# Optimization experiments

Hardware: AMD Instinct MI355X
Metric: run time of the kernel (lower is better)

## Reference

```python
import jax, jax.numpy as jnp
import numpy as np

OMIC_SIZES = [89, 334, 534, 471, 1510, 482]
N = 8192      # number of WSI patches
DIN = 384     # input patch feature dim
DH = 512      # dim_hidden
H = 256       # SNN hidden dim ('small')
K = 6         # topk


def _leaky(x):
    return jnp.where(x >= 0, x, 0.01 * x)


def _elu(x):
    return jnp.where(x > 0, x, jnp.expm1(x))


def setup_inputs() -> dict:
    key = jax.random.key(0)
    ks = iter(jax.random.split(key, 64))
    d = {}
    for i, s in enumerate(OMIC_SIZES, 1):
        d[f'x_omic{i}'] = jax.random.normal(next(ks), (s,), jnp.float32)
        d[f'sig_w1_{i}'] = jax.random.normal(next(ks), (H, s), jnp.float32) * 0.05
    d['x_path'] = jax.random.normal(next(ks), (N, DIN), jnp.float32)
    d['sig_b1'] = jax.random.normal(next(ks), (6, H), jnp.float32) * 0.05
    d['sig_w2'] = jax.random.normal(next(ks), (6, H, H), jnp.float32) * 0.05
    d['sig_b2'] = jax.random.normal(next(ks), (6, H), jnp.float32) * 0.05
    d['fc1_w'] = jax.random.normal(next(ks), (DH, DIN), jnp.float32) * 0.05
    d['fc1_b'] = jax.random.normal(next(ks), (DH,), jnp.float32) * 0.05
    d['wh_w'] = jax.random.normal(next(ks), (DH, DH), jnp.float32) * 0.05
    d['wh_b'] = jax.random.normal(next(ks), (DH,), jnp.float32) * 0.05
    d['wt_w'] = jax.random.normal(next(ks), (DH, DH), jnp.float32) * 0.05
    d['wt_b'] = jax.random.normal(next(ks), (DH,), jnp.float32) * 0.05
    d['lin1_w'] = jax.random.normal(next(ks), (DH, DH), jnp.float32) * 0.05
    d['lin1_b'] = jax.random.normal(next(ks), (DH,), jnp.float32) * 0.05
    d['lin2_w'] = jax.random.normal(next(ks), (DH, DH), jnp.float32) * 0.05
    d['lin2_b'] = jax.random.normal(next(ks), (DH,), jnp.float32) * 0.05
    d['att_w1'] = jax.random.normal(next(ks), (DH // 2, DH), jnp.float32) * 0.05
    d['att_b1'] = jax.random.normal(next(ks), (DH // 2,), jnp.float32) * 0.05
    d['att_w2'] = jax.random.normal(next(ks), (1, DH // 2), jnp.float32) * 0.05
    d['att_b2'] = jax.random.normal(next(ks), (1,), jnp.float32) * 0.05
    return d


def _forward(x_omic1, x_omic2, x_omic3, x_omic4, x_omic5, x_omic6,
             sig_w1_1, sig_w1_2, sig_w1_3, sig_w1_4, sig_w1_5, sig_w1_6,
             sig_b1, sig_w2, sig_b2, x_path,
             fc1_w, fc1_b, wh_w, wh_b, wt_w, wt_b,
             lin1_w, lin1_b, lin2_w, lin2_b,
             att_w1, att_b1, att_w2, att_b2):
    # --- omic SNN branches (Linear+ELU x2; AlphaDropout is identity at eval) ---
    xo = [x_omic1, x_omic2, x_omic3, x_omic4, x_omic5, x_omic6]
    w1 = [sig_w1_1, sig_w1_2, sig_w1_3, sig_w1_4, sig_w1_5, sig_w1_6]
    eo = []
    for i in range(6):
        h = _elu(xo[i] @ w1[i].T + sig_b1[i])
        h = _elu(h @ sig_w2[i].T + sig_b2[i])
        eo.append(h)
    e_omic = jnp.stack(eo)[:, None, :]            # [6,1,256]

    # --- pathology branch ---
    h = _leaky(x_path @ fc1_w.T + fc1_b)[None]    # [1,N,DH]
    h = (h + h.mean(axis=1, keepdims=True)) * 0.5
    e_h = h @ wh_w.T + wh_b                       # [1,N,DH]
    e_t = h @ wt_w.T + wt_b                       # [1,N,DH]

    logits = (e_h * (DH ** -0.5)) @ jnp.swapaxes(e_t, -2, -1)  # [1,N,N]
    vals, idx = jax.lax.top_k(logits, K)          # [1,N,K]
    p = jax.nn.softmax(vals, axis=2)              # [1,N,K]
    Nb = e_t[0][idx[0]][None]                     # gather neighbors [1,N,K,DH]

    eh_r = p[..., None] * Nb + (1.0 - p)[..., None] * e_h[:, :, None, :]
    gate = jnp.tanh(e_h[:, :, None, :] + eh_r)    # [1,N,K,DH]
    # faithful to einsum('ijkl,ijkm->ijk'): separable sums over l and m
    ka = Nb.sum(-1) * gate.sum(-1)                # [1,N,K]
    kp = jax.nn.softmax(ka, axis=2)
    e_Nh = jnp.einsum('bnk,bnkd->bnd', kp, Nb)    # [1,N,DH]

    s = _leaky((e_h + e_Nh) @ lin1_w.T + lin1_b)
    b = _leaky((e_h * e_Nh) @ lin2_w.T + lin2_b)
    e_h2 = s + b                                  # dropout is identity at eval

    # --- GlobalAttention readout ---
    x = e_h2[0]                                   # [N,DH]
    g = _leaky(x @ att_w1.T + att_b1) @ att_w2.T + att_b2  # [N,1]
    a = jax.nn.softmax(g, axis=0)
    e_g = (a * x).sum(axis=0, keepdims=True)      # [1,DH]
    return e_omic, e_h2, e_g


def reference(x_omic1, x_omic2, x_omic3, x_omic4, x_omic5, x_omic6,
              sig_w1_1, sig_w1_2, sig_w1_3, sig_w1_4, sig_w1_5, sig_w1_6,
              sig_b1, sig_w2, sig_b2, x_path,
              fc1_w, fc1_b, wh_w, wh_b, wt_w, wt_b,
              lin1_w, lin1_b, lin2_w, lin2_b,
              att_w1, att_b1, att_w2, att_b2):
    return _forward(x_omic1, x_omic2, x_omic3, x_omic4, x_omic5, x_omic6,
                    sig_w1_1, sig_w1_2, sig_w1_3, sig_w1_4, sig_w1_5, sig_w1_6,
                    sig_b1, sig_w2, sig_b2, x_path,
                    fc1_w, fc1_b, wh_w, wh_b, wt_w, wt_b,
                    lin1_w, lin1_b, lin2_w, lin2_b,
                    att_w1, att_b1, att_w2, att_b2)
```

## Files before the change

kernel.cpp:

```cpp
#include <hip/hip_runtime.h>
#include <math.h>

typedef unsigned short u16;
typedef unsigned int u32;
typedef __attribute__((ext_vector_type(8))) short s8v;
typedef __attribute__((ext_vector_type(16))) float f16f;

__device__ __forceinline__ float b2f(u16 u){ union{u32 i; float f;} v; v.i=((u32)u)<<16; return v.f; }
__device__ __forceinline__ u16 f2b(float f){ union{float f; u32 i;} v; v.f=f; u32 x=v.i; return (u16)((x + 0x7fffu + ((x>>16)&1u)) >> 16); }
__device__ __forceinline__ float leakyf(float x){ return x>=0.f? x : 0.01f*x; }

#define MFMA32(a,b,c) __builtin_amdgcn_mfma_f32_32x32x16_bf16(a,b,c,0,0,0)

__device__ __forceinline__ void gl_lds16(const void* g, void* l){
    __builtin_amdgcn_global_load_lds(
        (const __attribute__((address_space(1))) u32*)g,
        (__attribute__((address_space(3))) u32*)l, 16, 0, 0);
}

struct OmicArgs {
    const float* x[6];
    const float* w1[6];
    int s[6];
};

__global__ __launch_bounds__(256) void omic_kernel(OmicArgs oa,
        const float* __restrict__ sb1, const float* __restrict__ sw2,
        const float* __restrict__ sb2, float* __restrict__ out)
{
    int br = blockIdx.x;
    int t = threadIdx.x;
    int s = oa.s[br];
    __shared__ float xs[1536];
    __shared__ float h1[256];
    const float* x = oa.x[br];
    for (int i=t;i<s;i+=256) xs[i] = x[i];
    __syncthreads();
    const float* w1r = oa.w1[br] + (size_t)t * s;
    float a = sb1[br*256+t];
    for (int i=0;i<s;++i) a += xs[i]*w1r[i];
    a = a>0.f ? a : expm1f(a);
    h1[t] = a;
    __syncthreads();
    const float* w2r = sw2 + (size_t)br*65536 + (size_t)t*256;
    float a2 = sb2[br*256+t];
    #pragma unroll 4
    for (int i=0;i<256;++i) a2 += h1[i]*w2r[i];
    a2 = a2>0.f ? a2 : expm1f(a2);
    out[br*256+t] = a2;
}

struct WcSeg { const float* s; u16* dh; u16* dl; int n; };
struct WcArgs { WcSeg seg[6]; };

__global__ __launch_bounds__(256) void wconv(WcArgs a)
{
    WcSeg sg = a.seg[blockIdx.y];
    for (int i = blockIdx.x*256 + threadIdx.x; i < sg.n; i += gridDim.x*256){
        float v = sg.s[i];
        u16 hi = f2b(v);
        sg.dh[i] = hi;
        if (sg.dl) sg.dl[i] = f2b(v - b2f(hi));
    }
}

template<int SPLITA, int OUTMODE>
__global__ __launch_bounds__(256,2) void gemm_mfma(
    const float* __restrict__ A, const u16* __restrict__ Wh, const u16* __restrict__ Wl,
    const float* __restrict__ bias,
    float* __restrict__ Cf, u16* __restrict__ Ch, u16* __restrict__ Cl,
    int M, int N, int K)
{
    __shared__ u16 Ash[4096], Asl[4096], Bsh[4096], Bsl[4096];
    int tid = threadIdx.x, w = tid >> 6, lane = tid & 63;
    int l31 = lane & 31, l5 = lane >> 5, lo8 = lane << 3;
    int wr = w >> 1, wc = w & 1;
    int bm = blockIdx.x << 7, bn = blockIdx.y << 7;

    f16f acc[2][2];
    #pragma unroll
    for (int a0=0;a0<2;++a0)
        #pragma unroll
        for (int a1=0;a1<2;++a1)
            #pragma unroll
            for (int e=0;e<16;++e) acc[a0][a1][e] = 0.f;

    for (int k0 = 0; k0 < K; k0 += 32){
        __syncthreads();
        #pragma unroll
        for (int kf = 0; kf < 2; ++kf){
            int kk = k0 + (kf<<4) + (l5<<3);
            const float* ap = A + (size_t)(bm + (w<<5) + l31) * K + kk;
            float4 v0 = *(const float4*)ap;
            float4 v1 = *(const float4*)(ap + 4);
            float vv[8] = {v0.x,v0.y,v0.z,v0.w,v1.x,v1.y,v1.z,v1.w};
            s8v hv, lv;
            #pragma unroll
            for (int j=0;j<8;++j){
                u16 hi = f2b(vv[j]);
                hv[j] = (short)hi;
                if (SPLITA) lv[j] = (short)f2b(vv[j] - b2f(hi));
            }
            int fb = ((w<<1)+kf)<<9;
            *(s8v*)&Ash[fb + lo8] = hv;
            if (SPLITA) *(s8v*)&Asl[fb + lo8] = lv;
            size_t gb = (size_t)(bn + (w<<5) + l31) * K + kk;
            gl_lds16(Wh + gb, &Bsh[fb]);
            if (SPLITA) gl_lds16(Wl + gb, &Bsl[fb]);
        }
        __syncthreads();
        #pragma unroll
        for (int kf = 0; kf < 2; ++kf){
            s8v ah[2], al[2];
            #pragma unroll
            for (int rti=0;rti<2;++rti){
                int fa = (((((wr<<1)+rti)<<1)+kf)<<9) + lo8;
                ah[rti] = *(const s8v*)&Ash[fa];
                if (SPLITA) al[rti] = *(const s8v*)&Asl[fa];
            }
            #pragma unroll
            for (int cti=0;cti<2;++cti){
                int fb = (((((wc<<1)+cti)<<1)+kf)<<9) + lo8;
                s8v bh = *(const s8v*)&Bsh[fb];
                s8v bl;
                if (SPLITA) bl = *(const s8v*)&Bsl[fb];
                #pragma unroll
                for (int rti=0;rti<2;++rti){
                    acc[rti][cti] = MFMA32(ah[rti], bh, acc[rti][cti]);
                    if (SPLITA){
                        acc[rti][cti] = MFMA32(ah[rti], bl, acc[rti][cti]);
                        acc[rti][cti] = MFMA32(al[rti], bh, acc[rti][cti]);
                    }
                }
            }
        }
    }
    #pragma unroll
    for (int cti=0;cti<2;++cti){
        int col = bn + (((wc<<1)+cti)<<5) + l31;
        float bv = bias[col];
        #pragma unroll
        for (int rti=0;rti<2;++rti){
            int rbase = bm + (((wr<<1)+rti)<<5) + (l5<<2);
            #pragma unroll
            for (int g=0;g<4;++g){
                #pragma unroll
                for (int i=0;i<4;++i){
                    int row = rbase + (g<<3) + i;
                    float v = acc[rti][cti][(g<<2)+i] + bv;
                    if (OUTMODE==0){
                        Cf[(size_t)row*N + col] = leakyf(v);
                    } else {
                        u16 hi = f2b(v);
                        Ch[(size_t)row*N + col] = hi;
                        Cl[(size_t)row*N + col] = f2b(v - b2f(hi));
                    }
                }
            }
        }
    }
}

__global__ __launch_bounds__(256,2) void lin12_mfma(
    const u16* __restrict__ EHH, const u16* __restrict__ EHL, const u16* __restrict__ ENH,
    const u16* __restrict__ W1b, const float* __restrict__ B1,
    const u16* __restrict__ W2b, const float* __restrict__ B2,
    float* __restrict__ OUT)
{
    const int K = 512, N = 512;
    __shared__ u16 Ss[4096], Ms[4096], B1s[4096], B2s[4096];
    int tid = threadIdx.x, w = tid >> 6, lane = tid & 63;
    int l31 = lane & 31, l5 = lane >> 5, lo8 = lane << 3;
    int wr = w >> 1, wc = w & 1;
    int bm = blockIdx.x << 7, bn = blockIdx.y << 7;

    f16f acc1[2][2], acc2[2][2];
    #pragma unroll
    for (int a0=0;a0<2;++a0)
        #pragma unroll
        for (int a1=0;a1<2;++a1)
            #pragma unroll
            for (int e=0;e<16;++e){ acc1[a0][a1][e]=0.f; acc2[a0][a1][e]=0.f; }

    for (int k0 = 0; k0 < K; k0 += 32){
        __syncthreads();
        #pragma unroll
        for (int kf = 0; kf < 2; ++kf){
            int kk = k0 + (kf<<4) + (l5<<3);
            size_t go = (size_t)(bm + (w<<5) + l31) * K + kk;
            s8v hv = *(const s8v*)(EHH + go);
            s8v lv = *(const s8v*)(EHL + go);
            s8v nv = *(const s8v*)(ENH + go);
            s8v sv, mv;
            #pragma unroll
            for (int j=0;j<8;++j){
                float e = b2f((u16)hv[j]) + b2f((u16)lv[j]);
                float n = b2f((u16)nv[j]);
                sv[j] = (short)f2b(e + n);
                mv[j] = (short)f2b(e * n);
            }
            int fb = ((w<<1)+kf)<<9;
            *(s8v*)&Ss[fb + lo8] = sv;
            *(s8v*)&Ms[fb + lo8] = mv;
            size_t gb = (size_t)(bn + (w<<5) + l31) * K + kk;
            gl_lds16(W1b + gb, &B1s[fb]);
            gl_lds16(W2b + gb, &B2s[fb]);
        }
        __syncthreads();
        #pragma unroll
        for (int kf = 0; kf < 2; ++kf){
            s8v as[2], am[2];
            #pragma unroll
            for (int rti=0;rti<2;++rti){
                int fa = (((((wr<<1)+rti)<<1)+kf)<<9) + lo8;
                as[rti] = *(const s8v*)&Ss[fa];
                am[rti] = *(const s8v*)&Ms[fa];
            }
            #pragma unroll
            for (int cti=0;cti<2;++cti){
                int fb = (((((wc<<1)+cti)<<1)+kf)<<9) + lo8;
                s8v b1 = *(const s8v*)&B1s[fb];
                s8v b2 = *(const s8v*)&B2s[fb];
                #pragma unroll
                for (int rti=0;rti<2;++rti){
                    acc1[rti][cti] = MFMA32(as[rti], b1, acc1[rti][cti]);
                    acc2[rti][cti] = MFMA32(am[rti], b2, acc2[rti][cti]);
                }
            }
        }
    }
    #pragma unroll
    for (int cti=0;cti<2;++cti){
        int col = bn + (((wc<<1)+cti)<<5) + l31;
        float b1v = B1[col], b2v = B2[col];
        #pragma unroll
        for (int rti=0;rti<2;++rti){
            int rbase = bm + (((wr<<1)+rti)<<5) + (l5<<2);
            #pragma unroll
            for (int g=0;g<4;++g){
                #pragma unroll
                for (int i=0;i<4;++i){
                    int row = rbase + (g<<3) + i;
                    float s1 = leakyf(acc1[rti][cti][(g<<2)+i] + b1v);
                    float s2 = leakyf(acc2[rti][cti][(g<<2)+i] + b2v);
                    OUT[(size_t)row*N + col] = s1 + s2;
                }
            }
        }
    }
}

__global__ __launch_bounds__(256) void colmean(const float* __restrict__ H, float* __restrict__ Mc)
{
    __shared__ float red[256];
    int c=blockIdx.x, t=threadIdx.x;
    float s=0;
    for (int i=t;i<8192;i+=256) s += H[(size_t)i*512 + c];
    red[t]=s; __syncthreads();
    for (int o=128;o>0;o>>=1){ if(t<o) red[t]+=red[t+o]; __syncthreads(); }
    if (t==0) Mc[c] = red[0] * (1.0f/8192.0f);
}

__global__ __launch_bounds__(256) void hupd(float* __restrict__ H, const float* __restrict__ Mc)
{
    int i = blockIdx.x*256 + threadIdx.x;
    H[i] = (H[i] + Mc[i & 511]) * 0.5f;
}

struct TileMem { u16 Ah[8*512]; u16 Al[8*512]; u16 Bh[8*512]; u16 Bl[8*512]; };
struct EpiMem  { float Sc[64*132]; };
union SMemU { TileMem t; EpiMem e; };

__global__ __launch_bounds__(256,3) void logits_topk_mfma(
    const u16* __restrict__ EHH, const u16* __restrict__ EHL,
    const u16* __restrict__ ETH, const u16* __restrict__ ETL,
    float* __restrict__ VALS, int* __restrict__ IDX)
{
    const float scale = 0.04419417382415922f;
    __shared__ SMemU sm;
    int tid = threadIdx.x;
    int bm = blockIdx.x << 7;
    int base = blockIdx.y << 9;
    int w = tid >> 6, lane = tid & 63;
    int l31 = lane & 31, l5 = lane >> 5;
    int wr = w >> 1, wc = w & 1;
    int lo8 = lane << 3;
    int r = tid >> 1, q = tid & 1;

    float tv[6]; int ti[6];
    #pragma unroll
    for (int k=0;k<6;++k){ tv[k]=-INFINITY; ti[k]=0; }

    for (int bnoff = 0; bnoff < 512; bnoff += 128){
        int bn = base + bnoff;
        f16f acc[2][2];
        #pragma unroll
        for (int a0=0;a0<2;++a0)
            #pragma unroll
            for (int a1=0;a1<2;++a1)
                #pragma unroll
                for (int e=0;e<16;++e) acc[a0][a1][e] = 0.f;

        for (int k0 = 0; k0 < 512; k0 += 32){
            __syncthreads();
            #pragma unroll
            for (int kf = 0; kf < 2; ++kf){
                int ksub = k0 + (kf<<4) + (l5<<3);
                size_t ga = (size_t)(bm + (w<<5) + l31) * 512 + ksub;
                gl_lds16(EHH + ga, &sm.t.Ah[((w<<1)+kf)<<9]);
                gl_lds16(EHL + ga, &sm.t.Al[((w<<1)+kf)<<9]);
                size_t gb = (size_t)(bn + (w<<5) + l31) * 512 + ksub;
                gl_lds16(ETH + gb, &sm.t.Bh[((w<<1)+kf)<<9]);
                gl_lds16(ETL + gb, &sm.t.Bl[((w<<1)+kf)<<9]);
            }
            __syncthreads();
            #pragma unroll
            for (int kf = 0; kf < 2; ++kf){
                s8v ah[2], al[2];
                #pragma unroll
                for (int rti=0;rti<2;++rti){
                    int fa = (((((wr<<1)+rti)<<1)+kf)<<9) + lo8;
                    ah[rti] = *(const s8v*)&sm.t.Ah[fa];
                    al[rti] = *(const s8v*)&sm.t.Al[fa];
                }
                #pragma unroll
                for (int cti=0;cti<2;++cti){
                    int fb = (((((wc<<1)+cti)<<1)+kf)<<9) + lo8;
                    s8v bh = *(const s8v*)&sm.t.Bh[fb];
                    s8v bl = *(const s8v*)&sm.t.Bl[fb];
                    #pragma unroll
                    for (int rti=0;rti<2;++rti){
                        acc[rti][cti] = MFMA32(ah[rti], bh, acc[rti][cti]);
                        acc[rti][cti] = MFMA32(ah[rti], bl, acc[rti][cti]);
                        acc[rti][cti] = MFMA32(al[rti], bh, acc[rti][cti]);
                    }
                }
            }
        }
        __syncthreads();
        #pragma unroll
        for (int h = 0; h < 2; ++h){
            if (wc == h){
                #pragma unroll
                for (int cti=0;cti<2;++cti){
                    int colw = ((cti<<5) + l31) * 132 + (wr<<6) + (l5<<2);
                    #pragma unroll
                    for (int rti=0;rti<2;++rti){
                        #pragma unroll
                        for (int g=0;g<4;++g){
                            float4 vv;
                            vv.x = acc[rti][cti][(g<<2)+0]*scale;
                            vv.y = acc[rti][cti][(g<<2)+1]*scale;
                            vv.z = acc[rti][cti][(g<<2)+2]*scale;
                            vv.w = acc[rti][cti][(g<<2)+3]*scale;
                            *(float4*)&sm.e.Sc[colw + (rti<<5) + (g<<3)] = vv;
                        }
                    }
                }
            }
            __syncthreads();
            int cbase = bn + (h<<6) + (q<<5);
            #pragma unroll
            for (int i=0;i<32;++i){
                float v = sm.e.Sc[(((q<<5)+i)*132) + r];
                if (v > tv[5]){
                    tv[5]=v; ti[5]=cbase+i;
                    #pragma unroll
                    for (int u=5;u>0;--u){
                        if (tv[u] > tv[u-1]){
                            float tf=tv[u]; tv[u]=tv[u-1]; tv[u-1]=tf;
                            int tg=ti[u]; ti[u]=ti[u-1]; ti[u-1]=tg;
                        }
                    }
                }
            }
            __syncthreads();
        }
    }
    float* Mv = sm.e.Sc;
    int*   Mi = (int*)sm.e.Sc + 1536;
    #pragma unroll
    for (int k=0;k<6;++k){ Mv[r*12 + q*6 + k] = tv[k]; Mi[r*12 + q*6 + k] = ti[k]; }
    __syncthreads();
    if (tid < 128){
        int row = bm + tid;
        float* mv = &Mv[tid*12];
        int*   mi = &Mi[tid*12];
        unsigned used = 0;
        for (int k=0;k<6;++k){
            float bv=-INFINITY; int bc=0;
            for (int c=0;c<12;++c) if (!((used>>c)&1u) && mv[c] > bv){ bv=mv[c]; bc=c; }
            used |= 1u<<bc;
            VALS[(size_t)row*96 + blockIdx.y*6 + k] = bv;
            IDX [(size_t)row*96 + blockIdx.y*6 + k] = mi[bc];
        }
    }
}

__global__ __launch_bounds__(256) void knn_agg(
    const u16* __restrict__ EHH, const u16* __restrict__ EHL,
    const u16* __restrict__ ETH, const u16* __restrict__ ETL,
    const float* __restrict__ VALS, const int* __restrict__ IDX,
    u16* __restrict__ ENH)
{
    int wave = threadIdx.x >> 6, lane = threadIdx.x & 63;
    int row = (blockIdx.x<<2) + wave;
    size_t vb = (size_t)row*96;
    float v0 = VALS[vb + lane];
    float v1 = (lane < 32) ? VALS[vb + 64 + lane] : -INFINITY;
    int e0 = lane, e1 = 64 + lane;
    float v[6]; int id[6];
    #pragma unroll
    for (int k=0;k<6;++k){
        float cv; int ce;
        if (v0 >= v1){ cv=v0; ce=e0; } else { cv=v1; ce=e1; }
        #pragma unroll
        for (int off=1; off<64; off<<=1){
            float ov = __shfl_xor(cv, off, 64);
            int   oe = __shfl_xor(ce, off, 64);
            if (ov > cv || (ov == cv && oe < ce)){ cv=ov; ce=oe; }
        }
        v[k] = cv;
        id[k] = IDX[vb + ce];
        if (e0 == ce) v0 = -INFINITY;
        if (e1 == ce) v1 = -INFINITY;
    }
    float mx=v[0];
    #pragma unroll
    for (int k=1;k<6;++k) mx=fmaxf(mx,v[k]);
    float p[6], se=0.f;
    #pragma unroll
    for (int k=0;k<6;++k){ p[k]=expf(v[k]-mx); se+=p[k]; }
    float inv=1.f/se;
    #pragma unroll
    for (int k=0;k<6;++k) p[k]*=inv;

    size_t ro = (size_t)row*512;
    float e[8];
    #pragma unroll
    for (int j=0;j<8;++j){ int o = lane + (j<<6); e[j]=b2f(EHH[ro+o])+b2f(EHL[ro+o]); }
    float nb[6][8], sn[6], sg[6];
    #pragma unroll
    for (int k=0;k<6;++k){
        size_t no = (size_t)id[k]*512;
        float s_n=0.f, s_g=0.f;
        #pragma unroll
        for (int j=0;j<8;++j){
            int o = lane + (j<<6);
            float nv = b2f(ETH[no+o])+b2f(ETL[no+o]);
            nb[k][j]=nv;
            s_n += nv;
            float ehr_v = p[k]*nv + (1.f-p[k])*e[j];
            s_g += tanhf(e[j] + ehr_v);
        }
        #pragma unroll
        for (int o=1;o<64;o<<=1){ s_n += __shfl_xor(s_n,o,64); s_g += __shfl_xor(s_g,o,64); }
        sn[k]=s_n; sg[k]=s_g;
    }
    float ka[6];
    #pragma unroll
    for (int k=0;k<6;++k) ka[k]=sn[k]*sg[k];
    float km=ka[0];
    #pragma unroll
    for (int k=1;k<6;++k) km=fmaxf(km,ka[k]);
    float kp[6], ks=0.f;
    #pragma unroll
    for (int k=0;k<6;++k){ kp[k]=expf(ka[k]-km); ks+=kp[k]; }
    float kinv=1.f/ks;
    #pragma unroll
    for (int k=0;k<6;++k) kp[k]*=kinv;
    float o8[8]={0,0,0,0,0,0,0,0};
    #pragma unroll
    for (int k=0;k<6;++k)
        #pragma unroll
        for (int j=0;j<8;++j) o8[j] += kp[k]*nb[k][j];
    #pragma unroll
    for (int j=0;j<8;++j) ENH[ro + lane + (j<<6)] = f2b(o8[j]);
}

__global__ __launch_bounds__(256) void att_g(
    const float* __restrict__ HM, const float* __restrict__ W2,
    const float* __restrict__ B2, float* __restrict__ G)
{
    int wave=threadIdx.x>>6, lane=threadIdx.x&63;
    int row=(blockIdx.x<<2)+wave;
    const float* hr = HM + (size_t)row*256;
    float s=0.f;
    #pragma unroll
    for (int j=0;j<4;++j) s += hr[lane+(j<<6)] * W2[lane+(j<<6)];
    #pragma unroll
    for (int o=1;o<64;o<<=1) s += __shfl_xor(s,o,64);
    if (lane==0) G[row] = s + B2[0];
}

__global__ __launch_bounds__(1024) void softg(float* __restrict__ G)
{
    __shared__ float red[1024];
    __shared__ float MS[2];
    int t=threadIdx.x;
    float m=-INFINITY;
    for (int i=t;i<8192;i+=1024) m=fmaxf(m,G[i]);
    red[t]=m; __syncthreads();
    for (int o=512;o>0;o>>=1){ if(t<o) red[t]=fmaxf(red[t],red[t+o]); __syncthreads(); }
    if (t==0) MS[0]=red[0];
    __syncthreads();
    float M=MS[0], s=0.f;
    for (int i=t;i<8192;i+=1024) s += expf(G[i]-M);
    red[t]=s; __syncthreads();
    for (int o=512;o>0;o>>=1){ if(t<o) red[t]+=red[t+o]; __syncthreads(); }
    if (t==0) MS[1]=red[0];
    __syncthreads();
    float inv=1.f/MS[1];
    for (int i=t;i<8192;i+=1024) G[i] = expf(G[i]-M)*inv;
}

__global__ __launch_bounds__(256) void eg_kernel(
    const float* __restrict__ A, const float* __restrict__ X, float* __restrict__ OUT)
{
    __shared__ float red[256];
    int d = blockIdx.x, t = threadIdx.x;
    float s=0.f;
    for (int i=t;i<8192;i+=256) s += A[i]*X[(size_t)i*512 + d];
    red[t]=s; __syncthreads();
    for (int o=128;o>0;o>>=1){ if(t<o) red[t]+=red[t+o]; __syncthreads(); }
    if (t==0) OUT[d] = red[0];
}

extern "C" void kernel_launch(void* const* d_in, const int* in_sizes, int n_in,
                              void* d_out, int out_size, void* d_ws, size_t ws_size,
                              hipStream_t stream)
{
    (void)n_in; (void)out_size; (void)ws_size;
    static const int ss[6] = {89,334,534,471,1510,482};

    bool sig_order = (in_sizes[12] == 1536);
    OmicArgs oa;
    const float *sb1, *sw2, *sb2, *xpath;
    if (sig_order) {
        for (int i=0;i<6;++i){ oa.x[i]=(const float*)d_in[i]; oa.w1[i]=(const float*)d_in[6+i]; oa.s[i]=ss[i]; }
        sb1   = (const float*)d_in[12];
        sw2   = (const float*)d_in[13];
        sb2   = (const float*)d_in[14];
        xpath = (const float*)d_in[15];
    } else {
        for (int i=0;i<6;++i){ oa.x[i]=(const float*)d_in[2*i]; oa.w1[i]=(const float*)d_in[2*i+1]; oa.s[i]=ss[i]; }
        xpath = (const float*)d_in[12];
        sb1   = (const float*)d_in[13];
        sw2   = (const float*)d_in[14];
        sb2   = (const float*)d_in[15];
    }
    const float* fc1w = (const float*)d_in[16];
    const float* fc1b = (const float*)d_in[17];
    const float* whw  = (const float*)d_in[18];
    const float* whb  = (const float*)d_in[19];
    const float* wtw  = (const float*)d_in[20];
    const float* wtb  = (const float*)d_in[21];
    const float* l1w  = (const float*)d_in[22];
    const float* l1b  = (const float*)d_in[23];
    const float* l2w  = (const float*)d_in[24];
    const float* l2b  = (const float*)d_in[25];
    const float* aw1  = (const float*)d_in[26];
    const float* ab1  = (const float*)d_in[27];
    const float* aw2  = (const float*)d_in[28];
    const float* ab2  = (const float*)d_in[29];

    float* out = (float*)d_out;
    float* eh2 = out + 1536;
    float* egp = out + 1536 + 4194304;

    float* h    = eh2;
    float* vals = eh2;
    int*   idxb = (int*)(eh2 + 786432);

    char* wsb = (char*)d_ws;
    u16* ehh = (u16*)wsb;
    u16* ehl = ehh + 4194304;
    u16* eth = ehl + 4194304;
    u16* etl = eth + 4194304;
    u16* enh = etl + 4194304;
    u16* wreg = enh + 4194304;
    u16* fc1h = wreg,            *fc1l = wreg +  196608;
    u16* whh  = wreg +  393216,  *whl  = wreg +  655360;
    u16* wth  = wreg +  917504,  *wtl  = wreg + 1179648;
    u16* l1bf = wreg + 1441792,  *l2bf = wreg + 1703936;
    u16* awbf = wreg + 1966080;
    float* mcol = (float*)(wsb + 48234496);
    float* gbuf = mcol + 512;
    float* hm   = (float*)eth;

    omic_kernel<<<6,256,0,stream>>>(oa, sb1, sw2, sb2, out);

    WcArgs wa;
    wa.seg[0] = { fc1w, fc1h, fc1l, 196608 };
    wa.seg[1] = { whw,  whh,  whl,  262144 };
    wa.seg[2] = { wtw,  wth,  wtl,  262144 };
    wa.seg[3] = { l1w,  l1bf, nullptr, 262144 };
    wa.seg[4] = { l2w,  l2bf, nullptr, 262144 };
    wa.seg[5] = { aw1,  awbf, nullptr, 131072 };
    wconv<<<dim3(16,6),256,0,stream>>>(wa);

    gemm_mfma<1,0><<<dim3(64,4),256,0,stream>>>(xpath, fc1h, fc1l, fc1b, h, nullptr, nullptr, 8192,512,384);
    colmean<<<512,256,0,stream>>>(h, mcol);
    hupd<<<16384,256,0,stream>>>(h, mcol);
    gemm_mfma<1,1><<<dim3(64,4),256,0,stream>>>(h, whh, whl, whb, nullptr, ehh, ehl, 8192,512,512);
    gemm_mfma<1,1><<<dim3(64,4),256,0,stream>>>(h, wth, wtl, wtb, nullptr, eth, etl, 8192,512,512);
    logits_topk_mfma<<<dim3(64,16),256,0,stream>>>(ehh, ehl, eth, etl, vals, idxb);
    knn_agg<<<2048,256,0,stream>>>(ehh, ehl, eth, etl, vals, idxb, enh);
    lin12_mfma<<<dim3(64,4),256,0,stream>>>(ehh, ehl, enh, l1bf, l1b, l2bf, l2b, eh2);
    gemm_mfma<0,0><<<dim3(64,2),256,0,stream>>>(eh2, awbf, awbf, ab1, hm, nullptr, nullptr, 8192,256,512);
    att_g<<<2048,256,0,stream>>>(hm, aw2, ab2, gbuf);
    softg<<<1,1024,0,stream>>>(gbuf);
    eg_kernel<<<512,256,0,stream>>>(gbuf, eh2, egp);
}
```

Measured before the change: 918.6 us.

## Widen logits tile to 128x256 and halve top-k column splits

The logits+topk kernel now computes 128x256 output tiles (4 column subtiles per wave) and covers 1024 columns per block, so the grid's y dimension drops from 16 to 8. The A fragments are reused across twice as many B columns, which cuts global loads of the row operand. The partial top-k buffer shrinks from 96 to 48 candidates per row, so knn_agg's merge handles a single 48-entry lane set. In exchange, accumulator registers and LDS use roughly double, and occupancy is lowered to 2 blocks per SM.

```diff
diff --git a/kernel.cpp b/kernel.cpp
--- a/kernel.cpp
+++ b/kernel.cpp
@@ -267,11 +267,11 @@
     H[i] = (H[i] + Mc[i & 511]) * 0.5f;
 }
 
-struct TileMem { u16 Ah[8*512]; u16 Al[8*512]; u16 Bh[8*512]; u16 Bl[8*512]; };
+struct TileMem { u16 Ah[4096]; u16 Al[4096]; u16 Bh[8192]; u16 Bl[8192]; };
 struct EpiMem  { float Sc[64*132]; };
 union SMemU { TileMem t; EpiMem e; };
 
-__global__ __launch_bounds__(256,3) void logits_topk_mfma(
+__global__ __launch_bounds__(256,2) void logits_topk_mfma(
     const u16* __restrict__ EHH, const u16* __restrict__ EHL,
     const u16* __restrict__ ETH, const u16* __restrict__ ETL,
     float* __restrict__ VALS, int* __restrict__ IDX)
@@ -280,24 +280,23 @@
     __shared__ SMemU sm;
     int tid = threadIdx.x;
     int bm = blockIdx.x << 7;
-    int base = blockIdx.y << 9;
+    int base = blockIdx.y << 10;
     int w = tid >> 6, lane = tid & 63;
-    int l31 = lane & 31, l5 = lane >> 5;
+    int l31 = lane & 31, l5 = lane >> 5, lo8 = lane << 3;
     int wr = w >> 1, wc = w & 1;
-    int lo8 = lane << 3;
     int r = tid >> 1, q = tid & 1;
 
     float tv[6]; int ti[6];
     #pragma unroll
     for (int k=0;k<6;++k){ tv[k]=-INFINITY; ti[k]=0; }
 
-    for (int bnoff = 0; bnoff < 512; bnoff += 128){
-        int bn = base + bnoff;
-        f16f acc[2][2];
+    for (int bt = 0; bt < 4; ++bt){
+        int bn = base + (bt<<8);
+        f16f acc[2][4];
         #pragma unroll
         for (int a0=0;a0<2;++a0)
             #pragma unroll
-            for (int a1=0;a1<2;++a1)
+            for (int a1=0;a1<4;++a1)
                 #pragma unroll
                 for (int e=0;e<16;++e) acc[a0][a1][e] = 0.f;
 
@@ -305,13 +304,17 @@
             __syncthreads();
             #pragma unroll
             for (int kf = 0; kf < 2; ++kf){
-                int ksub = k0 + (kf<<4) + (l5<<3);
-                size_t ga = (size_t)(bm + (w<<5) + l31) * 512 + ksub;
+                int kk = k0 + (kf<<4) + (l5<<3);
+                size_t ga = (size_t)(bm + (w<<5) + l31) * 512 + kk;
                 gl_lds16(EHH + ga, &sm.t.Ah[((w<<1)+kf)<<9]);
                 gl_lds16(EHL + ga, &sm.t.Al[((w<<1)+kf)<<9]);
-                size_t gb = (size_t)(bn + (w<<5) + l31) * 512 + ksub;
-                gl_lds16(ETH + gb, &sm.t.Bh[((w<<1)+kf)<<9]);
-                gl_lds16(ETL + gb, &sm.t.Bl[((w<<1)+kf)<<9]);
+                #pragma unroll
+                for (int j = 0; j < 2; ++j){
+                    int ct = (w<<1) + j;
+                    size_t gb = (size_t)(bn + (ct<<5) + l31) * 512 + kk;
+                    gl_lds16(ETH + gb, &sm.t.Bh[((ct<<1)+kf)<<9]);
+                    gl_lds16(ETL + gb, &sm.t.Bl[((ct<<1)+kf)<<9]);
+                }
             }
             __syncthreads();
             #pragma unroll
@@ -324,8 +327,8 @@
                     al[rti] = *(const s8v*)&sm.t.Al[fa];
                 }
                 #pragma unroll
-                for (int cti=0;cti<2;++cti){
-                    int fb = (((((wc<<1)+cti)<<1)+kf)<<9) + lo8;
+                for (int cti=0;cti<4;++cti){
+                    int fb = (((((wc<<2)+cti)<<1)+kf)<<9) + lo8;
                     s8v bh = *(const s8v*)&sm.t.Bh[fb];
                     s8v bl = *(const s8v*)&sm.t.Bl[fb];
                     #pragma unroll
@@ -339,11 +342,12 @@
         }
         __syncthreads();
         #pragma unroll
-        for (int h = 0; h < 2; ++h){
-            if (wc == h){
-                #pragma unroll
-                for (int cti=0;cti<2;++cti){
-                    int colw = ((cti<<5) + l31) * 132 + (wr<<6) + (l5<<2);
+        for (int s = 0; s < 4; ++s){
+            if (wc == (s>>1)){
+                #pragma unroll
+                for (int cp=0;cp<2;++cp){
+                    int cti = ((s&1)<<1) + cp;
+                    int colw = ((cp<<5) + l31) * 132 + (wr<<6) + (l5<<2);
                     #pragma unroll
                     for (int rti=0;rti<2;++rti){
                         #pragma unroll
@@ -359,7 +363,7 @@
                 }
             }
             __syncthreads();
-            int cbase = bn + (h<<6) + (q<<5);
+            int cbase = bn + (s<<6) + (q<<5);
             #pragma unroll
             for (int i=0;i<32;++i){
                 float v = sm.e.Sc[(((q<<5)+i)*132) + r];
@@ -391,8 +395,8 @@
             float bv=-INFINITY; int bc=0;
             for (int c=0;c<12;++c) if (!((used>>c)&1u) && mv[c] > bv){ bv=mv[c]; bc=c; }
             used |= 1u<<bc;
-            VALS[(size_t)row*96 + blockIdx.y*6 + k] = bv;
-            IDX [(size_t)row*96 + blockIdx.y*6 + k] = mi[bc];
+            VALS[(size_t)row*48 + blockIdx.y*6 + k] = bv;
+            IDX [(size_t)row*48 + blockIdx.y*6 + k] = mi[bc];
         }
     }
 }
@@ -405,15 +409,13 @@
 {
     int wave = threadIdx.x >> 6, lane = threadIdx.x & 63;
     int row = (blockIdx.x<<2) + wave;
-    size_t vb = (size_t)row*96;
-    float v0 = VALS[vb + lane];
-    float v1 = (lane < 32) ? VALS[vb + 64 + lane] : -INFINITY;
-    int e0 = lane, e1 = 64 + lane;
+    size_t vb = (size_t)row*48;
+    float v0 = (lane < 48) ? VALS[vb + lane] : -INFINITY;
+    int e0 = lane;
     float v[6]; int id[6];
     #pragma unroll
     for (int k=0;k<6;++k){
-        float cv; int ce;
-        if (v0 >= v1){ cv=v0; ce=e0; } else { cv=v1; ce=e1; }
+        float cv = v0; int ce = e0;
         #pragma unroll
         for (int off=1; off<64; off<<=1){
             float ov = __shfl_xor(cv, off, 64);
@@ -423,7 +425,6 @@
         v[k] = cv;
         id[k] = IDX[vb + ce];
         if (e0 == ce) v0 = -INFINITY;
-        if (e1 == ce) v1 = -INFINITY;
     }
     float mx=v[0];
     #pragma unroll
@@ -599,15 +600,19 @@
     wa.seg[5] = { aw1,  awbf, nullptr, 131072 };
     wconv<<<dim3(16,6),256,0,stream>>>(wa);
 
-    gemm_mfma<1,0><<<dim3(64,4),256,0,stream>>>(xpath, fc1h, fc1l, fc1b, h, nullptr, nullptr, 8192,512,384);
+    gemm_mfma<1,0><<<dim3(64,4),256,0,stream>>>(xpath, fc1h, fc1l, fc1b,
+        h, nullptr, nullptr, 8192,512,384);
     colmean<<<512,256,0,stream>>>(h, mcol);
     hupd<<<16384,256,0,stream>>>(h, mcol);
-    gemm_mfma<1,1><<<dim3(64,4),256,0,stream>>>(h, whh, whl, whb, nullptr, ehh, ehl, 8192,512,512);
-    gemm_mfma<1,1><<<dim3(64,4),256,0,stream>>>(h, wth, wtl, wtb, nullptr, eth, etl, 8192,512,512);
-    logits_topk_mfma<<<dim3(64,16),256,0,stream>>>(ehh, ehl, eth, etl, vals, idxb);
+    gemm_mfma<1,1><<<dim3(64,4),256,0,stream>>>(h, whh, whl, whb,
+        nullptr, ehh, ehl, 8192,512,512);
+    gemm_mfma<1,1><<<dim3(64,4),256,0,stream>>>(h, wth, wtl, wtb,
+        nullptr, eth, etl, 8192,512,512);
+    logits_topk_mfma<<<dim3(64,8),256,0,stream>>>(ehh, ehl, eth, etl, vals, idxb);
     knn_agg<<<2048,256,0,stream>>>(ehh, ehl, eth, etl, vals, idxb, enh);
     lin12_mfma<<<dim3(64,4),256,0,stream>>>(ehh, ehl, enh, l1bf, l1b, l2bf, l2b, eh2);
-    gemm_mfma<0,0><<<dim3(64,2),256,0,stream>>>(eh2, awbf, awbf, ab1, hm, nullptr, nullptr, 8192,256,512);
+    gemm_mfma<0,0><<<dim3(64,2),256,0,stream>>>(eh2, awbf, awbf, ab1,
+        hm, nullptr, nullptr, 8192,256,512);
     att_g<<<2048,256,0,stream>>>(hm, aw2, ab2, gbuf);
     softg<<<1,1024,0,stream>>>(gbuf);
     eg_kernel<<<512,256,0,stream>>>(gbuf, eh2, egp);
```

After: 829.3 us. 9.7% less time.
